# Performance work log

Hardware: AMD Instinct MI355X
Metric: run time of the kernel (lower is better)

The kernel has to match this reference:

```python
import jax, jax.numpy as jnp
import numpy as np

HEADS = 4


def rel_to_abs(x):
    """Convert relative logits [..., L, 2L-1] to absolute [..., L, L].
    out[..., i, j] = x[..., i, j - i + L - 1]."""
    L = x.shape[-2]
    idx = jnp.arange(L)[None, :] - jnp.arange(L)[:, None] + (L - 1)  # [L, L]
    idx = jnp.broadcast_to(idx, x.shape[:-1] + (L,))
    return jnp.take_along_axis(x, idx, axis=-1)


def setup_inputs() -> dict:
    key = jax.random.key(0)
    ks = jax.random.split(key, 5)
    b, c, h, w = 2, 256, 64, 64
    dh = c // HEADS
    return {
        "x": jax.random.normal(ks[0], (b, c, h, w), jnp.float32),
        "w_qkv": jax.random.normal(ks[1], (3 * c, c), jnp.float32) / np.float32(np.sqrt(c)),
        "w_out": jax.random.normal(ks[2], (c, c), jnp.float32) / np.float32(np.sqrt(c)),
        "rel_height": jax.random.normal(ks[3], (2 * h - 1, dh), jnp.float32),
        "rel_width": jax.random.normal(ks[4], (2 * w - 1, dh), jnp.float32),
    }


def reference(x, w_qkv, w_out, rel_height, rel_width):
    b, c, h, w = x.shape
    dh = c // HEADS
    N = h * w
    scale = dh ** -0.5

    # 1x1 conv == per-pixel matmul over channels
    qkv = jnp.einsum('bchw,oc->bohw', x, w_qkv)  # [b, 3c, h, w]
    q, k, v = jnp.split(qkv, 3, axis=1)

    def to_heads(t):  # [b, c, h, w] -> [b, H, N, dh]
        return t.reshape(b, HEADS, dh, N).transpose(0, 1, 3, 2)

    q = to_heads(q) * scale
    k = to_heads(k)
    v = to_heads(v)

    # content-content scores over spatial positions
    content = jnp.einsum('bnid,bnjd->bnij', q, k)  # [b, H, N, N]

    q5 = q.reshape(b, HEADS, h, w, dh)  # [b, H, x, y, dh]
    # width relative logits: [b,H,x,y,2w-1] -> abs -> [b,H,x,y,jw]
    rw = rel_to_abs(jnp.einsum('bnxyd,rd->bnxyr', q5, rel_width))
    # height relative logits on transposed spatial: [b,H,y,x,2h-1] -> [b,H,y,x,jh]
    rh = rel_to_abs(jnp.einsum('bnyxd,rd->bnyxr', q5.transpose(0, 1, 3, 2, 4), rel_height))

    logits = content.reshape(b, HEADS, h, w, h, w)
    logits = logits + rw[:, :, :, :, None, :]  # broadcast width bias over target height jh
    logits = logits + rh.transpose(0, 1, 3, 2, 4)[:, :, :, :, :, None]  # [b,H,x,y,jh] over jw

    attn = jax.nn.softmax(logits.reshape(b, HEADS, N, N), axis=-1)
    out = jnp.einsum('bnij,bnjd->bnid', attn, v)  # [b, H, N, dh]
    out = out.transpose(0, 1, 3, 2).reshape(b, c, h, w)
    out = jnp.einsum('bchw,oc->bohw', out, w_out)  # 1x1 out projection
    return out + x
```

## Files before the change

kernel.cpp:

```cpp
#include <hip/hip_runtime.h>

typedef unsigned short u16;
typedef unsigned int u32;
typedef __bf16 bf16x8 __attribute__((ext_vector_type(8)));
typedef __bf16 bf16x2 __attribute__((ext_vector_type(2)));
typedef float f32x4 __attribute__((ext_vector_type(4)));
typedef float f32x2 __attribute__((ext_vector_type(2)));
typedef u32 u32x4 __attribute__((ext_vector_type(4)));
typedef u32 u32x2 __attribute__((ext_vector_type(2)));
typedef short s16x4 __attribute__((ext_vector_type(4)));

#define DEVI __device__ __forceinline__

#if defined(__has_builtin)
#if __has_builtin(__builtin_amdgcn_exp2f)
#define EXP2F(x) __builtin_amdgcn_exp2f(x)
#endif
#endif
#ifndef EXP2F
#define EXP2F(x) exp2f(x)
#endif

#define MFMA16(a, b, c) __builtin_amdgcn_mfma_f32_16x16x32_bf16(a, b, c, 0, 0, 0)
#define MFMA1K(a, b, c) __builtin_amdgcn_mfma_f32_16x16x16bf16_1k(a, b, c, 0, 0, 0)

typedef __attribute__((address_space(1))) u32 gu32;
typedef __attribute__((address_space(3))) u32 lu32;
DEVI void gll16(const u16* g, u16* l) {
    __builtin_amdgcn_global_load_lds((const gu32*)g, (lu32*)l, 16, 0, 0);
}
#define WAIT_VM0() __builtin_amdgcn_s_waitcnt(0x0f70)

DEVI u16 f2bf(float f) {
    u32 u = __builtin_bit_cast(u32, f);
    u = (u + 0x7FFFu + ((u >> 16) & 1u)) >> 16;
    return (u16)u;
}
DEVI float bf2f(u16 h) {
    u32 u = ((u32)h) << 16;
    return __builtin_bit_cast(float, u);
}
DEVI float bfhi(u32 u) { return __builtin_bit_cast(float, u & 0xFFFF0000u); }
DEVI float bflo(u32 u) { return __builtin_bit_cast(float, u << 16); }
DEVI bf16x8 bc8(u32x4 u) { return __builtin_bit_cast(bf16x8, u); }
DEVI s16x4 bc4(u32 a, u32 b) {
    u32x2 v = {a, b};
    return __builtin_bit_cast(s16x4, v);
}
DEVI u32 pack2(float a, float b) {
    f32x2 v = {a, b};
    bf16x2 h = __builtin_convertvector(v, bf16x2);
    return __builtin_bit_cast(u32, h);
}

#define QSCALE 0.18033688011112042f

__global__ __launch_bounds__(256) void k_prep(const float* __restrict__ x,
                                              const float* __restrict__ wq,
                                              const float* __restrict__ wo,
                                              const float* __restrict__ relh,
                                              const float* __restrict__ relw,
                                              u16* __restrict__ xt, u16* __restrict__ wqb,
                                              u16* __restrict__ wob, u16* __restrict__ relhb,
                                              u16* __restrict__ relwb) {
    int bid = blockIdx.x;
    int t = threadIdx.x;
    if (bid < 512) {
        int pm = bid & 63, cm = (bid >> 6) & 3, b = bid >> 8;
        int p0 = pm * 64, c0 = cm * 64;
        __shared__ float tile[64][65];
#pragma unroll
        for (int it = 0; it < 4; ++it) {
            int idx = it * 256 + t;
            int cl = idx >> 4, f4 = idx & 15;
            f32x4 v = *(const f32x4*)(x + ((size_t)(b * 256 + c0 + cl)) * 4096 + p0 + f4 * 4);
            tile[cl][f4 * 4 + 0] = v[0];
            tile[cl][f4 * 4 + 1] = v[1];
            tile[cl][f4 * 4 + 2] = v[2];
            tile[cl][f4 * 4 + 3] = v[3];
        }
        __syncthreads();
#pragma unroll
        for (int it = 0; it < 2; ++it) {
            int idx = it * 256 + t;
            int pl = idx >> 3, g = idx & 7;
            u32x4 pk;
            pk.x = pack2(tile[g * 8 + 0][pl], tile[g * 8 + 1][pl]);
            pk.y = pack2(tile[g * 8 + 2][pl], tile[g * 8 + 3][pl]);
            pk.z = pack2(tile[g * 8 + 4][pl], tile[g * 8 + 5][pl]);
            pk.w = pack2(tile[g * 8 + 6][pl], tile[g * 8 + 7][pl]);
            *(u32x4*)(xt + ((size_t)(b * 4096 + p0 + pl)) * 256 + c0 + g * 8) = pk;
        }
    } else {
        int i0 = (bid - 512) * 256 + t;
#pragma unroll
        for (int i = i0; i < 196608; i += 65536) wqb[i] = f2bf(wq[i]);
        if (i0 < 65536) wob[i0] = f2bf(wo[i0]);
        if (i0 < 8192) {
            relhb[i0] = (i0 < 8128) ? f2bf(relh[i0]) : (u16)0;
            relwb[i0] = (i0 < 8128) ? f2bf(relw[i0]) : (u16)0;
        }
    }
}

__global__ __launch_bounds__(256) void k_qkv(const u16* __restrict__ xt, const u16* __restrict__ wqb,
                                             const u16* __restrict__ relwb,
                                             const u16* __restrict__ relhb,
                                             u16* __restrict__ q, u16* __restrict__ k,
                                             u16* __restrict__ vt, u16* __restrict__ Wabs,
                                             u16* __restrict__ HabsT) {
    int pm = blockIdx.x, on = blockIdx.y, b = blockIdx.z;
    int p0 = pm * 64, o0 = on * 64;
    __shared__ __align__(16) u16 Sm[64 * 256];
    int t = threadIdx.x;
    int wv = t >> 6, l = t & 63, quad = l >> 4, li = l & 15;

    u32x4 areg[8];
    const u32x4* arow = (const u32x4*)(xt + ((size_t)(b * 4096 + p0 + wv * 16 + li)) * 256);
#pragma unroll
    for (int kc = 0; kc < 8; ++kc) areg[kc] = arow[kc * 4 + quad];

    {
        int pc = l & 31;
#pragma unroll
        for (int i = 0; i < 8; ++i) {
            int r = wv * 16 + i * 2 + (l >> 5);
            gll16(wqb + (size_t)(o0 + r) * 256 + ((pc + r) & 31) * 8,
                  Sm + (wv * 16 + i * 2) * 256);
        }
    }
    WAIT_VM0();
    __syncthreads();

    f32x4 acc[4] = {{0, 0, 0, 0}, {0, 0, 0, 0}, {0, 0, 0, 0}, {0, 0, 0, 0}};
#pragma unroll
    for (int kc = 0; kc < 8; ++kc) {
        bf16x8 a = bc8(areg[kc]);
#pragma unroll
        for (int ct = 0; ct < 4; ++ct) {
            bf16x8 bb = bc8(*(const u32x4*)(Sm + (ct * 16 + li) * 256 +
                                            (((kc * 4 + quad) - (ct * 16 + li)) & 31) * 8));
            acc[ct] = MFMA16(a, bb, acc[ct]);
        }
    }

    int tensor = on >> 2, head = on & 3;
    if (tensor == 2) {
        __syncthreads();
        u16* T = Sm;
#pragma unroll
        for (int ct = 0; ct < 4; ++ct)
#pragma unroll
            for (int r = 0; r < 4; ++r)
                T[(ct * 16 + li) * 72 + wv * 16 + quad * 4 + r] = f2bf(acc[ct][r]);
        __syncthreads();
        int dr = t >> 2, pc = (t & 3) * 16;
        u32x4* g = (u32x4*)(vt + ((size_t)((b * 4 + head) * 64 + dr)) * 4096 + p0 + pc);
        const u32x4* s2 = (const u32x4*)(T + dr * 72 + pc);
        g[0] = s2[0];
        g[1] = s2[1];
    } else {
        u16* outp = (tensor == 0) ? q : k;
        float sc = (tensor == 0) ? QSCALE : 1.0f;
#pragma unroll
        for (int ct = 0; ct < 4; ++ct)
#pragma unroll
            for (int r = 0; r < 4; ++r) {
                int p = p0 + wv * 16 + quad * 4 + r;
                int d = ct * 16 + li;
                outp[((size_t)((b * 4 + head) * 4096 + p)) * 64 + d] = f2bf(acc[ct][r] * sc);
            }
        if (tensor == 0) {
            int bh = b * 4 + head;
            u16* T = Sm;
            u16* Ls = Sm + 64 * 72;
            __syncthreads();
#pragma unroll
            for (int ct = 0; ct < 4; ++ct)
#pragma unroll
                for (int r = 0; r < 4; ++r)
                    T[(wv * 16 + quad * 4 + r) * 72 + ct * 16 + li] = f2bf(acc[ct][r] * QSCALE);
            {
                int row = t >> 1, half = t & 1;
                const u32x4* g2 = (const u32x4*)(relwb + row * 64 + half * 32);
                u32x4* s2 = (u32x4*)(Ls + row * 72 + half * 32);
#pragma unroll
                for (int kk = 0; kk < 4; ++kk) s2[kk] = g2[kk];
            }
            __syncthreads();
            u32x4 aq2[2];
            aq2[0] = *(const u32x4*)(T + (wv * 16 + li) * 72 + quad * 8);
            aq2[1] = *(const u32x4*)(T + (wv * 16 + li) * 72 + 32 + quad * 8);

            f32x4 acc2[8];
#pragma unroll
            for (int ct = 0; ct < 8; ++ct) acc2[ct] = (f32x4){0.f, 0.f, 0.f, 0.f};
#pragma unroll
            for (int kc = 0; kc < 2; ++kc) {
                bf16x8 a = bc8(aq2[kc]);
#pragma unroll
                for (int ct = 0; ct < 8; ++ct) {
                    bf16x8 bb = bc8(*(const u32x4*)(Ls + (ct * 16 + li) * 72 + kc * 32 + quad * 8));
                    acc2[ct] = MFMA16(a, bb, acc2[ct]);
                }
            }
#pragma unroll
            for (int ct = 0; ct < 8; ++ct)
#pragma unroll
                for (int r = 0; r < 4; ++r) {
                    int row = wv * 16 + quad * 4 + r;
                    int j = (ct * 16 + li) - 63 + row;
                    if (j >= 0 && j < 64)
                        Wabs[((size_t)(bh * 4096 + p0 + row)) * 64 + j] = f2bf(acc2[ct][r]);
                }
            __syncthreads();
            {
                int row = t >> 1, half = t & 1;
                const u32x4* g2 = (const u32x4*)(relhb + row * 64 + half * 32);
                u32x4* s2 = (u32x4*)(Ls + row * 72 + half * 32);
#pragma unroll
                for (int kk = 0; kk < 4; ++kk) s2[kk] = g2[kk];
            }
            __syncthreads();
#pragma unroll
            for (int ct = 0; ct < 8; ++ct) acc2[ct] = (f32x4){0.f, 0.f, 0.f, 0.f};
#pragma unroll
            for (int kc = 0; kc < 2; ++kc) {
                bf16x8 a = bc8(aq2[kc]);
#pragma unroll
                for (int ct = 0; ct < 8; ++ct) {
                    bf16x8 bb = bc8(*(const u32x4*)(Ls + (ct * 16 + li) * 72 + kc * 32 + quad * 8));
                    acc2[ct] = MFMA16(a, bb, acc2[ct]);
                }
            }
#pragma unroll
            for (int ct = 0; ct < 8; ++ct)
#pragma unroll
                for (int r = 0; r < 4; ++r) {
                    int row = wv * 16 + quad * 4 + r;
                    int j = (ct * 16 + li) - 63 + pm;
                    if (j >= 0 && j < 64)
                        HabsT[((size_t)(bh * 64 + j)) * 4096 + p0 + row] = f2bf(acc2[ct][r]);
                }
        }
    }
}

__global__ __launch_bounds__(256, 2) void k_flash(const u16* __restrict__ q,
                                                  const u16* __restrict__ kg,
                                                  const u16* __restrict__ vt,
                                                  const u16* __restrict__ Wabs,
                                                  const u16* __restrict__ HabsT,
                                                  u16* __restrict__ OP,
                                                  float* __restrict__ LS) {
    int pm = blockIdx.x, bh = blockIdx.y, ks = blockIdx.z;
    int p0 = pm * 128;
    __shared__ __align__(16) u16 Kt[2][64 * 72];
    __shared__ __align__(16) u16 Vl[2][64 * 72];
    int t = threadIdx.x, wv = t >> 6, l = t & 63, quad = l >> 4, li = l & 15;
    int rbase = wv * 32;

    u32x4 aq[2][2];
#pragma unroll
    for (int rs = 0; rs < 2; ++rs) {
        const u32x4* qrow =
            (const u32x4*)(q + ((size_t)(bh * 4096 + p0 + rbase + rs * 16 + li)) * 64);
        aq[rs][0] = qrow[quad];
        aq[rs][1] = qrow[4 + quad];
    }

    f32x4 wb4[2][4];
#pragma unroll
    for (int rs = 0; rs < 2; ++rs)
#pragma unroll
        for (int ct = 0; ct < 4; ++ct) {
            const u32* wp = (const u32*)(Wabs +
                                         ((size_t)(bh * 4096 + p0 + rbase + rs * 16 + li)) * 64 +
                                         ct * 16 + quad * 4);
            u32 lo = wp[0], hi = wp[1];
            wb4[rs][ct] = (f32x4){bflo(lo), bfhi(lo), bflo(hi), bfhi(hi)};
        }

    const u16* hbase = HabsT + ((size_t)(bh * 64 + ks * 16)) * 4096 + p0 + rbase;

    int srow = t >> 2, scc = (t & 3) * 16, jt4 = (t & 3) * 4;
    {
        int j0 = ks * 1024;
        const u32x4* gk = (const u32x4*)(kg + ((size_t)(bh * 4096 + j0 + srow)) * 64 + scc);
        u32x4* sk = (u32x4*)(Kt[0] + srow * 72 + scc);
        sk[0] = gk[0];
        sk[1] = gk[1];
        const u32x4* gv = (const u32x4*)(vt + ((size_t)(bh * 64 + srow)) * 4096 + j0 + scc);
        u32x4 v0 = gv[0], v1 = gv[1];
        u16* vr = Vl[0] + srow * 72;
        *(u32x2*)(vr + jt4) = (u32x2){v0.x, v0.y};
        *(u32x2*)(vr + 16 + jt4) = (u32x2){v0.z, v0.w};
        *(u32x2*)(vr + 32 + jt4) = (u32x2){v1.x, v1.y};
        *(u32x2*)(vr + 48 + jt4) = (u32x2){v1.z, v1.w};
    }
    u16 hc0 = hbase[li];
    u16 hc1 = hbase[16 + li];

    f32x4 oacc[2][5];
#pragma unroll
    for (int rs = 0; rs < 2; ++rs)
#pragma unroll
        for (int ct = 0; ct < 5; ++ct) oacc[rs][ct] = (f32x4){0.f, 0.f, 0.f, 0.f};

    const s16x4 ones = {(short)0x3F80, (short)0x3F80, (short)0x3F80, (short)0x3F80};

    u32x4 kreg[2], vreg[2];
    u16 hn0, hn1;
    for (int kt = 0; kt < 16; ++kt) {
        __syncthreads();
        int cur = kt & 1;
        const u16* Kc = Kt[cur];
        const u16* Vc = Vl[cur];
        if (kt < 15) {
            int j0 = (ks * 16 + kt + 1) * 64;
            const u32x4* gk = (const u32x4*)(kg + ((size_t)(bh * 4096 + j0 + srow)) * 64 + scc);
            kreg[0] = gk[0];
            kreg[1] = gk[1];
            const u32x4* gv = (const u32x4*)(vt + ((size_t)(bh * 64 + srow)) * 4096 + j0 + scc);
            vreg[0] = gv[0];
            vreg[1] = gv[1];
            hn0 = hbase[(size_t)(kt + 1) * 4096 + li];
            hn1 = hbase[(size_t)(kt + 1) * 4096 + 16 + li];
        }

        float hh0 = bf2f(hc0);
        float hh1 = bf2f(hc1);
        f32x4 s[2][4];
#pragma unroll
        for (int ct = 0; ct < 4; ++ct) {
            s[0][ct] = wb4[0][ct] + hh0;
            s[1][ct] = wb4[1][ct] + hh1;
        }
#pragma unroll
        for (int kc = 0; kc < 2; ++kc) {
            bf16x8 b0 = bc8(aq[0][kc]), b1 = bc8(aq[1][kc]);
#pragma unroll
            for (int ct = 0; ct < 4; ++ct) {
                bf16x8 af = bc8(*(const u32x4*)(Kc + (ct * 16 + li) * 72 + kc * 32 + quad * 8));
                s[0][ct] = MFMA16(af, b0, s[0][ct]);
                s[1][ct] = MFMA16(af, b1, s[1][ct]);
            }
        }

        s16x4 pf[2][4];
#pragma unroll
        for (int rs = 0; rs < 2; ++rs)
#pragma unroll
            for (int ct = 0; ct < 4; ++ct) {
                u32x2 pp;
                pp.x = pack2(EXP2F(s[rs][ct][0]), EXP2F(s[rs][ct][1]));
                pp.y = pack2(EXP2F(s[rs][ct][2]), EXP2F(s[rs][ct][3]));
                pf[rs][ct] = __builtin_bit_cast(s16x4, pp);
            }

#pragma unroll
        for (int dt = 0; dt < 4; ++dt) {
            const u16* vr = Vc + (dt * 16 + li) * 72 + quad * 16;
            u32x4 B0 = *(const u32x4*)(vr);
            u32x4 B1 = *(const u32x4*)(vr + 8);
            s16x4 bv0 = bc4(B0.x, B0.y), bv1 = bc4(B0.z, B0.w);
            s16x4 bv2 = bc4(B1.x, B1.y), bv3 = bc4(B1.z, B1.w);
            oacc[0][dt] = MFMA1K(pf[0][0], bv0, oacc[0][dt]);
            oacc[1][dt] = MFMA1K(pf[1][0], bv0, oacc[1][dt]);
            oacc[0][dt] = MFMA1K(pf[0][1], bv1, oacc[0][dt]);
            oacc[1][dt] = MFMA1K(pf[1][1], bv1, oacc[1][dt]);
            oacc[0][dt] = MFMA1K(pf[0][2], bv2, oacc[0][dt]);
            oacc[1][dt] = MFMA1K(pf[1][2], bv2, oacc[1][dt]);
            oacc[0][dt] = MFMA1K(pf[0][3], bv3, oacc[0][dt]);
            oacc[1][dt] = MFMA1K(pf[1][3], bv3, oacc[1][dt]);
        }
#pragma unroll
        for (int jt = 0; jt < 4; ++jt) {
            oacc[0][4] = MFMA1K(pf[0][jt], ones, oacc[0][4]);
            oacc[1][4] = MFMA1K(pf[1][jt], ones, oacc[1][4]);
        }

        if (kt < 15) {
            u32x4* sk = (u32x4*)(Kt[cur ^ 1] + srow * 72 + scc);
            sk[0] = kreg[0];
            sk[1] = kreg[1];
            u16* vr = Vl[cur ^ 1] + srow * 72;
            *(u32x2*)(vr + jt4) = (u32x2){vreg[0].x, vreg[0].y};
            *(u32x2*)(vr + 16 + jt4) = (u32x2){vreg[0].z, vreg[0].w};
            *(u32x2*)(vr + 32 + jt4) = (u32x2){vreg[1].x, vreg[1].y};
            *(u32x2*)(vr + 48 + jt4) = (u32x2){vreg[1].z, vreg[1].w};
            hc0 = hn0;
            hc1 = hn1;
        }
    }

#pragma unroll
    for (int rs = 0; rs < 2; ++rs) {
#pragma unroll
        for (int ct = 0; ct < 4; ++ct)
#pragma unroll
            for (int r = 0; r < 4; ++r) {
                int p = p0 + rbase + rs * 16 + quad * 4 + r;
                OP[((size_t)((ks * 8 + bh) * 4096 + p)) * 64 + ct * 16 + li] =
                    f2bf(oacc[rs][ct][r]);
            }
        if (li == 0) {
#pragma unroll
            for (int r = 0; r < 4; ++r) {
                int p = p0 + rbase + rs * 16 + quad * 4 + r;
                LS[(size_t)(ks * 8 + bh) * 4096 + p] = oacc[rs][4][r];
            }
        }
    }
}

__global__ __launch_bounds__(256) void k_out2(const u16* __restrict__ wob,
                                              const u16* __restrict__ OP,
                                              const float* __restrict__ LS,
                                              const float* __restrict__ x,
                                              float* __restrict__ out) {
    int pm = blockIdx.x, b = blockIdx.y, coh = blockIdx.z;
    int p0 = pm * 64;
    __shared__ __align__(16) u16 Bt[64 * 264];
    int t = threadIdx.x, wv = t >> 6, l = t & 63, quad = l >> 4, li = l & 15;

    {
        int row = t >> 2, head = t & 3;
        int bh = b * 4 + head;
        int p = p0 + row;
        const u32x4* o0p = (const u32x4*)(OP + ((size_t)(bh * 4096 + p)) * 64);
        const u32x4* o1p = (const u32x4*)(OP + ((size_t)((8 + bh) * 4096 + p)) * 64);
        const u32x4* o2p = (const u32x4*)(OP + ((size_t)((16 + bh) * 4096 + p)) * 64);
        const u32x4* o3p = (const u32x4*)(OP + ((size_t)((24 + bh) * 4096 + p)) * 64);
        float linv = 1.0f / (LS[(size_t)bh * 4096 + p] + LS[(size_t)(8 + bh) * 4096 + p] +
                             LS[(size_t)(16 + bh) * 4096 + p] + LS[(size_t)(24 + bh) * 4096 + p]);
        u16* dst = Bt + row * 264 + head * 64;
#pragma unroll
        for (int kk = 0; kk < 8; ++kk) {
            u32x4 a = o0p[kk], c = o1p[kk], d = o2p[kk], e = o3p[kk];
            u32x4 pk;
            pk.x = pack2((bflo(a.x) + bflo(c.x) + bflo(d.x) + bflo(e.x)) * linv,
                         (bfhi(a.x) + bfhi(c.x) + bfhi(d.x) + bfhi(e.x)) * linv);
            pk.y = pack2((bflo(a.y) + bflo(c.y) + bflo(d.y) + bflo(e.y)) * linv,
                         (bfhi(a.y) + bfhi(c.y) + bfhi(d.y) + bfhi(e.y)) * linv);
            pk.z = pack2((bflo(a.z) + bflo(c.z) + bflo(d.z) + bflo(e.z)) * linv,
                         (bfhi(a.z) + bfhi(c.z) + bfhi(d.z) + bfhi(e.z)) * linv);
            pk.w = pack2((bflo(a.w) + bflo(c.w) + bflo(d.w) + bflo(e.w)) * linv,
                         (bfhi(a.w) + bfhi(c.w) + bfhi(d.w) + bfhi(e.w)) * linv);
            *(u32x4*)(dst + kk * 8) = pk;
        }
    }
    __syncthreads();

#pragma unroll
    for (int ci = 0; ci < 2; ++ci) {
        int com = coh * 2 + ci;
        int co0 = com * 64;
        f32x4 acc[4] = {{0, 0, 0, 0}, {0, 0, 0, 0}, {0, 0, 0, 0}, {0, 0, 0, 0}};
        const u32x4* arow = (const u32x4*)(wob + (size_t)(co0 + wv * 16 + li) * 256);
#pragma unroll
        for (int kc = 0; kc < 8; ++kc) {
            bf16x8 a = bc8(arow[kc * 4 + quad]);
#pragma unroll
            for (int ct = 0; ct < 4; ++ct) {
                bf16x8 bb = bc8(*(const u32x4*)(Bt + (ct * 16 + li) * 264 + kc * 32 + quad * 8));
                acc[ct] = MFMA16(a, bb, acc[ct]);
            }
        }
#pragma unroll
        for (int ct = 0; ct < 4; ++ct)
#pragma unroll
            for (int r = 0; r < 4; ++r) {
                size_t idx =
                    ((size_t)(b * 256 + co0 + wv * 16 + quad * 4 + r)) * 4096 + p0 + ct * 16 + li;
                out[idx] = acc[ct][r] + x[idx];
            }
    }
}

extern "C" void kernel_launch(void* const* d_in, const int* in_sizes, int n_in, void* d_out,
                              int out_size, void* d_ws, size_t ws_size, hipStream_t stream) {
    const float* x = (const float*)d_in[0];
    const float* wqkv = (const float*)d_in[1];
    const float* wout = (const float*)d_in[2];
    const float* relh = (const float*)d_in[3];
    const float* relw = (const float*)d_in[4];
    float* out = (float*)d_out;
    char* ws = (char*)d_ws;

    u16* xt = (u16*)(ws + 0);
    u16* wqb = (u16*)(ws + 4194304);
    u16* wob = (u16*)(ws + 4587520);
    u16* relwb = (u16*)(ws + 4718592);
    u16* relhb = (u16*)(ws + 4734976);
    u16* qb = (u16*)(ws + 4751360);
    u16* kb = (u16*)(ws + 8945664);
    u16* vtb = (u16*)(ws + 13139968);
    u16* Wabs = (u16*)(ws + 17334272);
    u16* HabsT = (u16*)(ws + 21528576);
    u16* OPart = (u16*)(ws + 25722880);
    float* LSum = (float*)(ws + 0);

    k_prep<<<768, 256, 0, stream>>>(x, wqkv, wout, relh, relw, xt, wqb, wob, relhb, relwb);
    k_qkv<<<dim3(64, 12, 2), 256, 0, stream>>>(xt, wqb, relwb, relhb, qb, kb, vtb, Wabs, HabsT);
    k_flash<<<dim3(32, 8, 4), 256, 0, stream>>>(qb, kb, vtb, Wabs, HabsT, OPart, LSum);
    k_out2<<<dim3(64, 2, 2), 256, 0, stream>>>(wob, OPart, LSum, x, out);
}
```

Baseline: 149.0 us.

## Replace 16x16x16 PV MFMAs with 16x16x32 via permuted K row layout

Permutes the order in which K rows are stored in shared memory so that the S accumulator layout of two adjacent column tiles matches the A-operand layout of the wider 16x16x32 bf16 MFMA. P·V and the row-sum MFMAs can then use half as many instructions, each with twice the K depth. V is now stored contiguously with 16-byte stores instead of scattered 8-byte ones. The bias column indexing (Wabs) is remapped to match the permutation, which adds some index arithmetic and depends on that remapping being correct.

```diff
diff --git a/kernel.cpp b/kernel.cpp
--- a/kernel.cpp
+++ b/kernel.cpp
@@ -8,7 +8,6 @@
 typedef float f32x2 __attribute__((ext_vector_type(2)));
 typedef u32 u32x4 __attribute__((ext_vector_type(4)));
 typedef u32 u32x2 __attribute__((ext_vector_type(2)));
-typedef short s16x4 __attribute__((ext_vector_type(4)));
 
 #define DEVI __device__ __forceinline__
 
@@ -22,7 +21,6 @@
 #endif
 
 #define MFMA16(a, b, c) __builtin_amdgcn_mfma_f32_16x16x32_bf16(a, b, c, 0, 0, 0)
-#define MFMA1K(a, b, c) __builtin_amdgcn_mfma_f32_16x16x16bf16_1k(a, b, c, 0, 0, 0)
 
 typedef __attribute__((address_space(1))) u32 gu32;
 typedef __attribute__((address_space(3))) u32 lu32;
@@ -43,10 +41,6 @@
 DEVI float bfhi(u32 u) { return __builtin_bit_cast(float, u & 0xFFFF0000u); }
 DEVI float bflo(u32 u) { return __builtin_bit_cast(float, u << 16); }
 DEVI bf16x8 bc8(u32x4 u) { return __builtin_bit_cast(bf16x8, u); }
-DEVI s16x4 bc4(u32 a, u32 b) {
-    u32x2 v = {a, b};
-    return __builtin_bit_cast(s16x4, v);
-}
 DEVI u32 pack2(float a, float b) {
     f32x2 v = {a, b};
     bf16x2 h = __builtin_convertvector(v, bf16x2);
@@ -274,29 +268,28 @@
     for (int rs = 0; rs < 2; ++rs)
 #pragma unroll
         for (int ct = 0; ct < 4; ++ct) {
+            int jcol = ((ct >> 1) * 32) + quad * 8 + ((ct & 1) * 4);
             const u32* wp = (const u32*)(Wabs +
                                          ((size_t)(bh * 4096 + p0 + rbase + rs * 16 + li)) * 64 +
-                                         ct * 16 + quad * 4);
+                                         jcol);
             u32 lo = wp[0], hi = wp[1];
             wb4[rs][ct] = (f32x4){bflo(lo), bfhi(lo), bflo(hi), bfhi(hi)};
         }
 
     const u16* hbase = HabsT + ((size_t)(bh * 64 + ks * 16)) * 4096 + p0 + rbase;
 
-    int srow = t >> 2, scc = (t & 3) * 16, jt4 = (t & 3) * 4;
+    int srow = t >> 2, scc = (t & 3) * 16;
+    int krow = ((srow >> 5) * 2 + ((srow >> 2) & 1)) * 16 + ((srow >> 3) & 3) * 4 + (srow & 3);
     {
         int j0 = ks * 1024;
         const u32x4* gk = (const u32x4*)(kg + ((size_t)(bh * 4096 + j0 + srow)) * 64 + scc);
-        u32x4* sk = (u32x4*)(Kt[0] + srow * 72 + scc);
+        u32x4* sk = (u32x4*)(Kt[0] + krow * 72 + scc);
         sk[0] = gk[0];
         sk[1] = gk[1];
         const u32x4* gv = (const u32x4*)(vt + ((size_t)(bh * 64 + srow)) * 4096 + j0 + scc);
-        u32x4 v0 = gv[0], v1 = gv[1];
-        u16* vr = Vl[0] + srow * 72;
-        *(u32x2*)(vr + jt4) = (u32x2){v0.x, v0.y};
-        *(u32x2*)(vr + 16 + jt4) = (u32x2){v0.z, v0.w};
-        *(u32x2*)(vr + 32 + jt4) = (u32x2){v1.x, v1.y};
-        *(u32x2*)(vr + 48 + jt4) = (u32x2){v1.z, v1.w};
+        u32x4* sv = (u32x4*)(Vl[0] + srow * 72 + scc);
+        sv[0] = gv[0];
+        sv[1] = gv[1];
     }
     u16 hc0 = hbase[li];
     u16 hc1 = hbase[16 + li];
@@ -307,7 +300,7 @@
 #pragma unroll
         for (int ct = 0; ct < 5; ++ct) oacc[rs][ct] = (f32x4){0.f, 0.f, 0.f, 0.f};
 
-    const s16x4 ones = {(short)0x3F80, (short)0x3F80, (short)0x3F80, (short)0x3F80};
+    const u32x4 ones = {0x3F803F80u, 0x3F803F80u, 0x3F803F80u, 0x3F803F80u};
 
     u32x4 kreg[2], vreg[2];
     u16 hn0, hn1;
@@ -347,48 +340,42 @@
             }
         }
 
-        s16x4 pf[2][4];
+        u32x4 pf[2][2];
 #pragma unroll
         for (int rs = 0; rs < 2; ++rs)
 #pragma unroll
-            for (int ct = 0; ct < 4; ++ct) {
-                u32x2 pp;
-                pp.x = pack2(EXP2F(s[rs][ct][0]), EXP2F(s[rs][ct][1]));
-                pp.y = pack2(EXP2F(s[rs][ct][2]), EXP2F(s[rs][ct][3]));
-                pf[rs][ct] = __builtin_bit_cast(s16x4, pp);
+            for (int p = 0; p < 2; ++p) {
+                u32x4 pp;
+                pp.x = pack2(EXP2F(s[rs][2 * p][0]), EXP2F(s[rs][2 * p][1]));
+                pp.y = pack2(EXP2F(s[rs][2 * p][2]), EXP2F(s[rs][2 * p][3]));
+                pp.z = pack2(EXP2F(s[rs][2 * p + 1][0]), EXP2F(s[rs][2 * p + 1][1]));
+                pp.w = pack2(EXP2F(s[rs][2 * p + 1][2]), EXP2F(s[rs][2 * p + 1][3]));
+                pf[rs][p] = pp;
             }
 
 #pragma unroll
         for (int dt = 0; dt < 4; ++dt) {
-            const u16* vr = Vc + (dt * 16 + li) * 72 + quad * 16;
+            const u16* vr = Vc + (dt * 16 + li) * 72 + quad * 8;
             u32x4 B0 = *(const u32x4*)(vr);
-            u32x4 B1 = *(const u32x4*)(vr + 8);
-            s16x4 bv0 = bc4(B0.x, B0.y), bv1 = bc4(B0.z, B0.w);
-            s16x4 bv2 = bc4(B1.x, B1.y), bv3 = bc4(B1.z, B1.w);
-            oacc[0][dt] = MFMA1K(pf[0][0], bv0, oacc[0][dt]);
-            oacc[1][dt] = MFMA1K(pf[1][0], bv0, oacc[1][dt]);
-            oacc[0][dt] = MFMA1K(pf[0][1], bv1, oacc[0][dt]);
-            oacc[1][dt] = MFMA1K(pf[1][1], bv1, oacc[1][dt]);
-            oacc[0][dt] = MFMA1K(pf[0][2], bv2, oacc[0][dt]);
-            oacc[1][dt] = MFMA1K(pf[1][2], bv2, oacc[1][dt]);
-            oacc[0][dt] = MFMA1K(pf[0][3], bv3, oacc[0][dt]);
-            oacc[1][dt] = MFMA1K(pf[1][3], bv3, oacc[1][dt]);
-        }
-#pragma unroll
-        for (int jt = 0; jt < 4; ++jt) {
-            oacc[0][4] = MFMA1K(pf[0][jt], ones, oacc[0][4]);
-            oacc[1][4] = MFMA1K(pf[1][jt], ones, oacc[1][4]);
+            u32x4 B1 = *(const u32x4*)(vr + 32);
+            oacc[0][dt] = MFMA16(bc8(pf[0][0]), bc8(B0), oacc[0][dt]);
+            oacc[1][dt] = MFMA16(bc8(pf[1][0]), bc8(B0), oacc[1][dt]);
+            oacc[0][dt] = MFMA16(bc8(pf[0][1]), bc8(B1), oacc[0][dt]);
+            oacc[1][dt] = MFMA16(bc8(pf[1][1]), bc8(B1), oacc[1][dt]);
+        }
+#pragma unroll
+        for (int p = 0; p < 2; ++p) {
+            oacc[0][4] = MFMA16(bc8(pf[0][p]), bc8(ones), oacc[0][4]);
+            oacc[1][4] = MFMA16(bc8(pf[1][p]), bc8(ones), oacc[1][4]);
         }
 
         if (kt < 15) {
-            u32x4* sk = (u32x4*)(Kt[cur ^ 1] + srow * 72 + scc);
+            u32x4* sk = (u32x4*)(Kt[cur ^ 1] + krow * 72 + scc);
             sk[0] = kreg[0];
             sk[1] = kreg[1];
-            u16* vr = Vl[cur ^ 1] + srow * 72;
-            *(u32x2*)(vr + jt4) = (u32x2){vreg[0].x, vreg[0].y};
-            *(u32x2*)(vr + 16 + jt4) = (u32x2){vreg[0].z, vreg[0].w};
-            *(u32x2*)(vr + 32 + jt4) = (u32x2){vreg[1].x, vreg[1].y};
-            *(u32x2*)(vr + 48 + jt4) = (u32x2){vreg[1].z, vreg[1].w};
+            u32x4* sv = (u32x4*)(Vl[cur ^ 1] + srow * 72 + scc);
+            sv[0] = vreg[0];
+            sv[1] = vreg[1];
             hc0 = hn0;
             hc1 = hn1;
         }
```

New measurement: 145.6 us. -2.3%, faster.
